# Kernel tuning notes

Measured on AMD Instinct MI355X. Metric: run time of the kernel, lower is better.

The kernel has to match this reference:

```python
import jax, jax.numpy as jnp
import numpy as np


def mish(x):
    return x * jnp.tanh(jax.nn.softplus(x))


def gcn(x, W, b, src, dst):
    # PyG GCNConv: h = D^-1/2 (A+I) D^-1/2 (x W) + b, aggregation at dst=edge_index[1]
    n = x.shape[0]
    h = x @ W
    deg = jax.ops.segment_sum(jnp.ones(src.shape[0], x.dtype), dst, num_segments=n) + 1.0
    dinv = jax.lax.rsqrt(deg)
    msg = h[src] * (dinv[src] * dinv[dst])[:, None]
    agg = jax.ops.segment_sum(msg, dst, num_segments=n)
    return agg + h * (dinv * dinv)[:, None] + b


def pool_mean(x, seg, num_segments):
    s = jax.ops.segment_sum(x, seg, num_segments=num_segments)
    c = jax.ops.segment_sum(jnp.ones(x.shape[0], x.dtype), seg, num_segments=num_segments)
    return s / jnp.maximum(c, 1.0)[:, None]


def attention(x, qW, qb, kW, kb, vW, vb, G):
    # x: [G*R, in_feats] -> per-graph self-attention over ROIs (dropout is identity in eval)
    R = x.shape[0] // G
    xc = x.reshape(G, R, x.shape[1])
    Q = xc @ qW + qb
    K = xc @ kW + kb
    Vv = xc @ vW + vb
    scores = jnp.einsum('gqd,gkd->gqk', Q, K) / (Q.shape[-1] ** 0.5)
    w = jax.nn.softmax(scores, axis=-1)
    out = jnp.einsum('gqk,gkd->gqd', w, Vv).reshape(G * R, Vv.shape[-1])
    return out, w.mean(axis=0)


def closs(a, b, temp=0.6):
    a = a / jnp.maximum(jnp.linalg.norm(a, axis=1, keepdims=True), 1e-12)
    b = b / jnp.maximum(jnp.linalg.norm(b, axis=1, keepdims=True), 1e-12)
    logits = (a @ b.T) / temp
    return -jnp.mean(jnp.diagonal(jax.nn.log_softmax(logits, axis=1)))


def setup_inputs() -> dict:
    key = jax.random.key(0)
    G, R1, R2, F_IN, H, OUT, DEG, V = 512, 200, 160, 128, 64, 64, 16, 64
    N1, N2 = G * R1, G * R2
    ks = iter(jax.random.split(key, 64))
    d = {}
    d['x1'] = jax.random.normal(next(ks), (N1, R1 + 3), jnp.float32)
    d['x2'] = jax.random.normal(next(ks), (N2, R2 + 3), jnp.float32)

    def lin(name, i, o):
        d[name + '_W'] = jax.random.normal(next(ks), (i, o), jnp.float32) * (i ** -0.5)
        d[name + '_b'] = jnp.zeros((o,), jnp.float32)

    lin('fcl', R1 + 3, F_IN); lin('fcr', R2 + 3, F_IN)
    lin('fcl1', R1, F_IN); lin('fcr1', R2, F_IN)
    lin('a1_q', F_IN, OUT); lin('a1_k', F_IN, OUT); lin('a1_v', F_IN, OUT)
    lin('a2_q', F_IN, OUT); lin('a2_k', F_IN, OUT); lin('a2_v', F_IN, OUT)
    lin('conv', F_IN, H); lin('conv1', H, H)
    lin('mlp', H, OUT)
    lin('fc1a', OUT * 4, F_IN); lin('fc1b', F_IN, 2)

    def edges(k, R):
        k1, k2 = jax.random.split(k)
        off = (jnp.arange(G, dtype=jnp.int32) * R)[:, None]
        src = jax.random.randint(k1, (G, R * DEG), 0, R, jnp.int32) + off
        dst = jax.random.randint(k2, (G, R * DEG), 0, R, jnp.int32) + off
        return jnp.stack([src.reshape(-1), dst.reshape(-1)])

    d['edge_index1'] = edges(next(ks), R1)
    d['edge_index2'] = edges(next(ks), R2)
    d['batch1'] = jnp.repeat(jnp.arange(G, dtype=jnp.int32), R1)
    d['batch2'] = jnp.repeat(jnp.arange(G, dtype=jnp.int32), R2)

    def sub(k, R):
        # one visited-node set (as in RW_subgraph) tiled per graph with offsets
        vis = jnp.sort(jax.random.permutation(k, R)[:V]).astype(jnp.int32)
        return (vis[None, :] + (jnp.arange(G, dtype=jnp.int32) * R)[:, None]).reshape(-1)

    d['sub_idx1'] = sub(next(ks), R1)
    d['sub_idx2'] = sub(next(ks), R2)
    d['num_graphs'] = G
    return d


def reference(x1, x2, fcl_W, fcl_b, fcr_W, fcr_b, fcl1_W, fcl1_b, fcr1_W, fcr1_b,
              a1_q_W, a1_q_b, a1_k_W, a1_k_b, a1_v_W, a1_v_b,
              a2_q_W, a2_q_b, a2_k_W, a2_k_b, a2_v_W, a2_v_b,
              conv_W, conv_b, conv1_W, conv1_b, mlp_W, mlp_b,
              fc1a_W, fc1a_b, fc1b_W, fc1b_b,
              edge_index1, edge_index2, batch1, batch2, sub_idx1, sub_idx2, num_graphs):
    G = int(num_graphs)
    src1, dst1 = edge_index1[0], edge_index1[1]
    src2, dst2 = edge_index2[0], edge_index2[1]

    z1 = x1[:, :-3] @ fcl1_W + fcl1_b
    z2 = x2[:, :-3] @ fcr1_W + fcr1_b
    z1, aw1 = attention(z1, a1_q_W, a1_q_b, a1_k_W, a1_k_b, a1_v_W, a1_v_b, G)
    z2, aw2 = attention(z2, a2_q_W, a2_q_b, a2_k_W, a2_k_b, a2_v_W, a2_v_b, G)
    z1 = pool_mean(z1, batch1, G)
    z2 = pool_mean(z2, batch2, G)

    h1 = x1 @ fcl_W + fcl_b
    h2 = x2 @ fcr_W + fcr_b
    o1 = mish(gcn(h1, conv_W, conv_b, src1, dst1))
    o2 = mish(gcn(h2, conv_W, conv_b, src2, dst2))
    o1 = gcn(o1, conv1_W, conv1_b, src1, dst1)
    o2 = gcn(o2, conv1_W, conv1_b, src2, dst2)

    s1 = o1[sub_idx1] @ mlp_W + mlp_b
    s2 = o2[sub_idx2] @ mlp_W + mlp_b
    s1 = pool_mean(s1, batch1[sub_idx1], G)
    s2 = pool_mean(s2, batch2[sub_idx2], G)

    c_loss = closs(s1, z2) + closs(z1, s2)
    feat = jnp.concatenate([s1, z1, s2, z2], axis=1)
    out = mish(feat @ fc1a_W + fc1a_b) @ fc1b_W + fc1b_b
    return c_loss, out, aw1, aw2
```

## Files before the change

kernel.cpp:

```cpp
#include <hip/hip_runtime.h>
#include <math.h>

#define TPB 256
#define MAXEP 4608

typedef float f32x4 __attribute__((ext_vector_type(4)));
typedef __bf16 bfv8 __attribute__((ext_vector_type(8)));

union U8 { uint4 q; unsigned short us[8]; __bf16 b[8]; bfv8 v; };

__device__ __forceinline__ unsigned short f2bfu(float f) {
  union { __bf16 h; unsigned short u; } x;
  x.h = (__bf16)f;
  return x.u;
}
__device__ __forceinline__ float bfu2f(unsigned short u) {
  return __uint_as_float((unsigned)u << 16);
}

__device__ __forceinline__ float mish_f(float x) {
  float sp = fmaxf(x, 0.f) + log1pf(expf(-fabsf(x)));
  return x * tanhf(sp);
}

__device__ __forceinline__ U8 loadA_f32(const float* Af, int kb, int K, bool rowok) {
  U8 u;
  if (rowok && kb + 8 <= K) {
    float4 f0 = *(const float4*)(Af + kb);
    float4 f1 = *(const float4*)(Af + kb + 4);
    u.b[0]=(__bf16)f0.x; u.b[1]=(__bf16)f0.y; u.b[2]=(__bf16)f0.z; u.b[3]=(__bf16)f0.w;
    u.b[4]=(__bf16)f1.x; u.b[5]=(__bf16)f1.y; u.b[6]=(__bf16)f1.z; u.b[7]=(__bf16)f1.w;
  } else {
#pragma unroll
    for (int j = 0; j < 8; ++j) {
      float f = (rowok && kb + j < K) ? Af[kb + j] : 0.f;
      u.b[j] = (__bf16)f;
    }
  }
  return u;
}

template<bool ABF16, bool CBF16, bool MISH, int NJ, int KPMAX, int RREP>
__global__ __launch_bounds__(256) void gemm2(
    const void* __restrict__ Av, const unsigned short* __restrict__ Bt,
    const float* __restrict__ bias, void* __restrict__ Cv,
    int N, int M, int K, int lda, int ldc,
    long sA, long sB, long sC, float alpha, int Kpad)
{
  constexpr int BM = NJ * 16;
  __shared__ unsigned short Bs[BM * KPMAX];

  const int tid = threadIdx.x;
  const int col0 = blockIdx.x * BM, row0 = blockIdx.y * 64 * RREP;

  {
    const unsigned short* Bp = Bt + (long)blockIdx.z * sB + (long)col0 * Kpad;
    int rows = M - col0; if (rows > BM) rows = BM;
    const int total = rows * Kpad;
    for (int i = tid * 8; i < total; i += TPB * 32) {
      uint4 a0, a1, a2, a3;
      bool b1 = i + TPB * 8  < total;
      bool b2 = i + TPB * 16 < total;
      bool b3 = i + TPB * 24 < total;
      a0 = *(const uint4*)&Bp[i];
      if (b1) a1 = *(const uint4*)&Bp[i + TPB * 8];
      if (b2) a2 = *(const uint4*)&Bp[i + TPB * 16];
      if (b3) a3 = *(const uint4*)&Bp[i + TPB * 24];
      *(uint4*)&Bs[i] = a0;
      if (b1) *(uint4*)&Bs[i + TPB * 8]  = a1;
      if (b2) *(uint4*)&Bs[i + TPB * 16] = a2;
      if (b3) *(uint4*)&Bs[i + TPB * 24] = a3;
    }
  }

  const int lane = tid & 63, w = tid >> 6;
  const int mrow = lane & 15, kg = lane >> 4;

  const unsigned short* Ah[RREP];
  const float* Af[RREP];
  bool rowok[RREP];
  U8 ua[RREP];
#pragma unroll
  for (int rr = 0; rr < RREP; ++rr) {
    int arow = row0 + rr * 64 + w * 16 + mrow;
    rowok[rr] = arow < N;
    if (ABF16) {
      Ah[rr] = (const unsigned short*)Av + (long)blockIdx.z * sA + (long)arow * lda;
      Af[rr] = nullptr;
      ua[rr].q = *(const uint4*)(Ah[rr] + kg * 8);
    } else {
      Af[rr] = (const float*)Av + (long)blockIdx.z * sA + (long)arow * lda;
      Ah[rr] = nullptr;
      ua[rr] = loadA_f32(Af[rr], kg * 8, K, rowok[rr]);
    }
  }

  __syncthreads();

  f32x4 acc[RREP][NJ];
#pragma unroll
  for (int rr = 0; rr < RREP; ++rr)
#pragma unroll
    for (int j = 0; j < NJ; ++j) acc[rr][j] = (f32x4)0.f;

  for (int k0 = 0; k0 < K; k0 += 32) {
    U8 un[RREP];
    bool more = (k0 + 32) < K;
    if (more) {
#pragma unroll
      for (int rr = 0; rr < RREP; ++rr) {
        if (ABF16) un[rr].q = *(const uint4*)(Ah[rr] + k0 + 32 + kg * 8);
        else       un[rr]   = loadA_f32(Af[rr], k0 + 32 + kg * 8, K, rowok[rr]);
      }
    }
    const int kb = k0 + kg * 8;
#pragma unroll
    for (int j = 0; j < NJ; ++j) {
      U8 ub;
      ub.q = *(const uint4*)&Bs[(j * 16 + mrow) * Kpad + kb];
#pragma unroll
      for (int rr = 0; rr < RREP; ++rr)
        acc[rr][j] = __builtin_amdgcn_mfma_f32_16x16x32_bf16(ua[rr].v, ub.v, acc[rr][j], 0, 0, 0);
    }
    if (more) {
#pragma unroll
      for (int rr = 0; rr < RREP; ++rr) ua[rr] = un[rr];
    }
  }

  long cbase = (long)blockIdx.z * sC;
#pragma unroll
  for (int rr = 0; rr < RREP; ++rr) {
#pragma unroll
    for (int j = 0; j < NJ; ++j) {
      int gc = col0 + j * 16 + mrow;
      if (gc >= M) continue;
      float bb = bias ? bias[gc] : 0.f;
#pragma unroll
      for (int r = 0; r < 4; ++r) {
        int gr = row0 + rr * 64 + w * 16 + kg * 4 + r;
        if (gr >= N) continue;
        float v = acc[rr][j][r] * alpha + bb;
        if (MISH) v = mish_f(v);
        if (CBF16) ((unsigned short*)Cv)[cbase + (long)gr * ldc + gc] = f2bfu(v);
        else       ((float*)Cv)[cbase + (long)gr * ldc + gc] = v;
      }
    }
  }
}

static inline int kpad_of(int K) { return ((K + 31) / 32) * 32 + 8; }

struct PrepSeg { const float* src; void* dst; int K, M, Kpad, kind; };
struct PrepArgs { PrepSeg s[19]; };

__global__ __launch_bounds__(256) void prep_weights(PrepArgs a) {
  PrepSeg sg = a.s[blockIdx.x];
  if (sg.kind == 0) {
    unsigned short* d = (unsigned short*)sg.dst;
    int tot = sg.M * sg.Kpad;
    for (int i = threadIdx.x; i < tot; i += TPB) {
      int m = i / sg.Kpad, k = i - m * sg.Kpad;
      float f = (k < sg.K) ? sg.src[(long)k * sg.M + m] : 0.f;
      d[i] = f2bfu(f);
    }
  } else if (sg.kind == 1) {
    float* d = (float*)sg.dst;
    for (int i = threadIdx.x; i < sg.K; i += TPB) d[i] = sg.src[i];
  } else {
    unsigned short* d = (unsigned short*)sg.dst;
    int tot = sg.M * sg.Kpad;
    for (int i = threadIdx.x; i < tot; i += TPB) {
      int m = i / sg.Kpad, k = i - m * sg.Kpad;
      float f = (k < sg.K) ? sg.src[(long)m * sg.K + k] : 0.f;
      d[i] = f2bfu(f);
    }
  }
}

__global__ __launch_bounds__(64) void bias_comb(const float* __restrict__ b_in,
                                                const unsigned short* __restrict__ Wt,
                                                int ldw, const float* __restrict__ bc,
                                                float* __restrict__ out, int M, int K)
{
  int m = blockIdx.x * 64 + threadIdx.x;
  if (m >= M) return;
  float s = bc ? bc[m] : 0.f;
  for (int k = 0; k < K; ++k) s += b_in[k] * bfu2f(Wt[(long)m * ldw + k]);
  out[m] = s;
}

__global__ __launch_bounds__(256) void ktvt2(
    const unsigned short* __restrict__ QKV, unsigned short* __restrict__ Kt,
    unsigned short* __restrict__ Vt, int R, int Rpad)
{
  __shared__ unsigned short tile[64][72];
  int g = blockIdx.x, tid = threadIdx.x;
  const unsigned short* q = QKV + (long)g * R * 192;
  unsigned short* kt = Kt + (long)g * R * 72;
  unsigned short* vt = Vt + (long)g * 64 * Rpad;

  {
    int c = tid & 63, w = tid >> 6;
    for (int r = w; r < R; r += 4)
      kt[r * 72 + c] = q[(long)r * 192 + 64 + c];
  }

  for (int r0 = 0; r0 < Rpad; r0 += 64) {
    __syncthreads();
    for (int i = tid; i < 64 * 64; i += TPB) {
      int rr = i >> 6, cc = i & 63;
      int r = r0 + rr;
      tile[cc][rr] = (r < R) ? q[(long)r * 192 + 128 + cc] : (unsigned short)0;
    }
    __syncthreads();
    int c = tid >> 2, j0 = (tid & 3) * 16;
    int lim = Rpad - r0; if (lim > 64) lim = 64;
    for (int jj = j0; jj < j0 + 16 && jj < lim; jj += 8) {
      uint4 qv = *(const uint4*)&tile[c][jj];
      *(uint4*)&vt[(long)c * Rpad + r0 + jj] = qv;
    }
  }
}

__global__ __launch_bounds__(256) void adj_build(
    const int* __restrict__ src, const int* __restrict__ dst,
    unsigned short* __restrict__ Adj, int R, int Rpad, int EPG)
{
  __shared__ float dinv_s[256];
  __shared__ unsigned short ssrc[MAXEP];
  __shared__ int cnt[256];
  __shared__ int scan[256];
  __shared__ int offx[257];
  __shared__ int cur[256];
  __shared__ float rowbuf[4][256];

  int g = blockIdx.x, tid = threadIdx.x;
  long ebase = (long)g * EPG;
  int gR = g * R;

  cnt[tid] = 0;
  __syncthreads();
  for (int e = tid; e < EPG; e += TPB)
    atomicAdd(&cnt[dst[ebase + e] - gR], 1);
  __syncthreads();

  int x = cnt[tid];
  int pc = (x + 7) & ~7;
  scan[tid] = pc;
  __syncthreads();
#pragma unroll
  for (int s = 1; s < 256; s <<= 1) {
    int t = (tid >= s) ? scan[tid - s] : 0;
    __syncthreads();
    scan[tid] += t;
    __syncthreads();
  }
  if (tid == 0) offx[0] = 0;
  offx[tid + 1] = scan[tid];
  cur[tid] = scan[tid] - pc;
  dinv_s[tid] = rsqrtf((float)x + 1.f);
  {
    unsigned dummy2 = 0xFFFFFFFFu;
    for (int i = tid; i < MAXEP / 2; i += TPB) ((unsigned*)ssrc)[i] = dummy2;
  }
  __syncthreads();

  for (int e = tid; e < EPG; e += TPB) {
    int d = dst[ebase + e] - gR;
    int s = src[ebase + e] - gR;
    int pos = atomicAdd(&cur[d], 1);
    ssrc[pos] = (unsigned short)s;
  }
  __syncthreads();

  int lane = tid & 63, w = tid >> 6;
  float* rb = rowbuf[w];
  for (int d = w; d < R; d += 4) {
#pragma unroll
    for (int i = 0; i < 4; ++i) rb[lane + i * 64] = 0.f;
    int i0 = offx[d], i1 = offx[d + 1];
    for (int i = i0 + lane; i < i1; i += 64) {
      int s = ssrc[i];
      if (s < R) atomicAdd(&rb[s], dinv_s[s]);
    }
    float dd = dinv_s[d];
    int c0 = lane * 4;
    if (c0 < Rpad) {
      ushort4 o;
      float v0 = rb[c0]     + (c0     == d ? dd : 0.f);
      float v1 = rb[c0 + 1] + (c0 + 1 == d ? dd : 0.f);
      float v2 = rb[c0 + 2] + (c0 + 2 == d ? dd : 0.f);
      float v3 = rb[c0 + 3] + (c0 + 3 == d ? dd : 0.f);
      o.x = f2bfu(v0 * dd); o.y = f2bfu(v1 * dd);
      o.z = f2bfu(v2 * dd); o.w = f2bfu(v3 * dd);
      *(ushort4*)&Adj[((long)gR + d) * Rpad + c0] = o;
    }
  }
}

__global__ __launch_bounds__(256) void transp64(
    const unsigned short* __restrict__ X, unsigned short* __restrict__ XT,
    int R, int Rpad)
{
  __shared__ unsigned short tile[64][72];
  int g = blockIdx.x, tid = threadIdx.x;
  const unsigned short* xg = X + (long)g * R * 64;
  unsigned short* xt = XT + (long)g * 64 * Rpad;
  for (int r0 = 0; r0 < Rpad; r0 += 64) {
    __syncthreads();
    for (int i = tid; i < 64 * 64; i += TPB) {
      int rr = i >> 6, cc = i & 63;
      int r = r0 + rr;
      tile[cc][rr] = (r < R) ? xg[(long)r * 64 + cc] : (unsigned short)0;
    }
    __syncthreads();
    int c = tid >> 2, j0 = (tid & 3) * 16;
    int lim = Rpad - r0; if (lim > 64) lim = 64;
    for (int jj = j0; jj < j0 + 16 && jj < lim; jj += 8) {
      uint4 q = *(const uint4*)&tile[c][jj];
      *(uint4*)&xt[(long)c * Rpad + r0 + jj] = q;
    }
  }
}

__global__ __launch_bounds__(256) void softmax_bf16(unsigned short* __restrict__ S,
                                                    int R, long rows)
{
  long wid = (long)blockIdx.x * 4 + (threadIdx.x >> 6);
  if (wid >= rows) return;
  int lane = threadIdx.x & 63;
  unsigned short* row = S + wid * R;
  float v[4];
  float mx = -1e30f;
#pragma unroll
  for (int t = 0; t < 4; ++t) {
    int j = lane + t * 64;
    v[t] = (j < R) ? bfu2f(row[j]) : -1e30f;
    mx = fmaxf(mx, v[t]);
  }
#pragma unroll
  for (int o = 32; o; o >>= 1) mx = fmaxf(mx, __shfl_xor(mx, o));
  float s = 0.f;
#pragma unroll
  for (int t = 0; t < 4; ++t) {
    int j = lane + t * 64;
    if (j < R) { v[t] = expf(v[t] - mx); s += v[t]; }
  }
#pragma unroll
  for (int o = 32; o; o >>= 1) s += __shfl_xor(s, o);
  float inv = 1.f / s;
#pragma unroll
  for (int t = 0; t < 4; ++t) {
    int j = lane + t * 64;
    if (j < R) row[j] = f2bfu(v[t] * inv);
  }
}

__global__ void meang_bf16(const unsigned short* __restrict__ S, float* __restrict__ out,
                           int RR, int G, float inv)
{
  int idx = blockIdx.x * TPB + threadIdx.x;
  if (idx >= RR) return;
  const unsigned short* p = S + idx;
  float s = 0.f;
  for (int g = 0; g + 8 <= G; g += 8) {
    s += bfu2f(p[(long)g * RR])       + bfu2f(p[(long)(g + 1) * RR]) +
         bfu2f(p[(long)(g + 2) * RR]) + bfu2f(p[(long)(g + 3) * RR]) +
         bfu2f(p[(long)(g + 4) * RR]) + bfu2f(p[(long)(g + 5) * RR]) +
         bfu2f(p[(long)(g + 6) * RR]) + bfu2f(p[(long)(g + 7) * RR]);
  }
  out[idx] = s * inv;
}

__global__ __launch_bounds__(256) void pool_mean_bf16(const unsigned short* __restrict__ X,
                                                      float* __restrict__ out, int R)
{
  __shared__ float part[4][64];
  int g = blockIdx.x, lane = threadIdx.x & 63, w = threadIdx.x >> 6;
  float s = 0.f;
  for (int r = w; r < R; r += 4)
    s += bfu2f(X[((long)g * R + r) * 64 + lane]);
  part[w][lane] = s;
  __syncthreads();
  if (w == 0)
    out[g * 64 + lane] = (part[0][lane] + part[1][lane] + part[2][lane] + part[3][lane]) * (1.f / R);
}

__global__ __launch_bounds__(64) void sub_mean_kernel(const unsigned short* __restrict__ X,
                                                      const int* __restrict__ sub,
                                                      float* __restrict__ out, int V)
{
  int g = blockIdx.x, lane = threadIdx.x;
  float s = 0.f;
  for (int v = 0; v + 4 <= V; v += 4) {
    int i0 = sub[g * V + v],     i1 = sub[g * V + v + 1];
    int i2 = sub[g * V + v + 2], i3 = sub[g * V + v + 3];
    s += bfu2f(X[(long)i0 * 64 + lane]) + bfu2f(X[(long)i1 * 64 + lane]) +
         bfu2f(X[(long)i2 * 64 + lane]) + bfu2f(X[(long)i3 * 64 + lane]);
  }
  out[g * 64 + lane] = s * (1.f / V);
}

__global__ __launch_bounds__(64) void norm_rows_kernel(const float* __restrict__ X,
                                                       float* __restrict__ Y)
{
  int g = blockIdx.x, lane = threadIdx.x;
  float x = X[g * 64 + lane];
  float ss = x * x;
#pragma unroll
  for (int o = 32; o; o >>= 1) ss += __shfl_xor(ss, o);
  float n = fmaxf(sqrtf(ss), 1e-12f);
  Y[g * 64 + lane] = x / n;
}

__global__ __launch_bounds__(256) void closs_kernel(const float* __restrict__ An,
                                                    const float* __restrict__ Bn,
                                                    float* __restrict__ loss, int G,
                                                    float invTemp, float coef)
{
  int i = blockIdx.x;
  __shared__ float arow[64];
  __shared__ float logits[512];
  __shared__ float red[256];
  int t = threadIdx.x;
  if (t < 64) arow[t] = An[i * 64 + t];
  __syncthreads();
  for (int j = t; j < G; j += 256) {
    const float* bp = Bn + (long)j * 64;
    float d = 0.f;
#pragma unroll
    for (int k = 0; k < 64; ++k) d = fmaf(arow[k], bp[k], d);
    logits[j] = d * invTemp;
  }
  __syncthreads();
  float mx = -1e30f;
  for (int j = t; j < G; j += 256) mx = fmaxf(mx, logits[j]);
  red[t] = mx; __syncthreads();
  for (int o = 128; o; o >>= 1) { if (t < o) red[t] = fmaxf(red[t], red[t + o]); __syncthreads(); }
  mx = red[0]; __syncthreads();
  float s = 0.f;
  for (int j = t; j < G; j += 256) s += expf(logits[j] - mx);
  red[t] = s; __syncthreads();
  for (int o = 128; o; o >>= 1) { if (t < o) red[t] += red[t + o]; __syncthreads(); }
  if (t == 0) {
    float lse = mx + logf(red[0]);
    atomicAdd(loss, coef * (lse - logits[i]));
  }
}

__global__ __launch_bounds__(128) void head_kernel(
    const float* __restrict__ s1, const float* __restrict__ z1,
    const float* __restrict__ s2, const float* __restrict__ z2,
    const float* __restrict__ W1, const float* __restrict__ b1,
    const float* __restrict__ W2, const float* __restrict__ b2,
    float* __restrict__ out)
{
  int g = blockIdx.x, t = threadIdx.x;
  __shared__ float feat[256];
  __shared__ float hid[128];
  if (t < 64) {
    feat[t]       = s1[g * 64 + t];
    feat[64 + t]  = z1[g * 64 + t];
    feat[128 + t] = s2[g * 64 + t];
    feat[192 + t] = z2[g * 64 + t];
  }
  __syncthreads();
  float acc = b1[t];
  for (int k = 0; k < 256; ++k) acc = fmaf(feat[k], W1[k * 128 + t], acc);
  hid[t] = mish_f(acc);
  __syncthreads();
  if (t < 2) {
    float a2 = b2[t];
#pragma unroll
    for (int k = 0; k < 128; ++k) a2 = fmaf(hid[k], W2[k * 2 + t], a2);
    out[g * 2 + t] = a2;
  }
}

#define LAUNCH_GEMM(ABF,CBF,MISH,NJ,KP,RREP, A,B,BI,C, N,M,K,LDA,LDC,SA,SB,SC,BAT,AL,KPAD) \
  { dim3 g_(((M)+(NJ)*16-1)/((NJ)*16), ((N)+(64*(RREP))-1)/(64*(RREP)), (BAT)); \
    gemm2<ABF,CBF,MISH,NJ,KP,RREP><<<g_,256,0,stream>>>((A),(B),(BI),(C),(N),(M),(K),(LDA),(LDC),(SA),(SB),(SC),(AL),(KPAD)); }

extern "C" void kernel_launch(void* const* d_in, const int* in_sizes, int n_in,
                              void* d_out, int out_size, void* d_ws, size_t ws_size,
                              hipStream_t stream)
{
  const float* x1     = (const float*)d_in[0];
  const float* x2     = (const float*)d_in[1];
  const float* fcl_W  = (const float*)d_in[2];  const float* fcl_b  = (const float*)d_in[3];
  const float* fcr_W  = (const float*)d_in[4];  const float* fcr_b  = (const float*)d_in[5];
  const float* fcl1_W = (const float*)d_in[6];  const float* fcl1_b = (const float*)d_in[7];
  const float* fcr1_W = (const float*)d_in[8];  const float* fcr1_b = (const float*)d_in[9];
  const float* a1qW = (const float*)d_in[10]; const float* a1qb = (const float*)d_in[11];
  const float* a1kW = (const float*)d_in[12]; const float* a1kb = (const float*)d_in[13];
  const float* a1vW = (const float*)d_in[14]; const float* a1vb = (const float*)d_in[15];
  const float* a2qW = (const float*)d_in[16]; const float* a2qb = (const float*)d_in[17];
  const float* a2kW = (const float*)d_in[18]; const float* a2kb = (const float*)d_in[19];
  const float* a2vW = (const float*)d_in[20]; const float* a2vb = (const float*)d_in[21];
  const float* convW  = (const float*)d_in[22]; const float* convb  = (const float*)d_in[23];
  const float* conv1W = (const float*)d_in[24]; const float* conv1b = (const float*)d_in[25];
  const float* mlpW   = (const float*)d_in[26]; const float* mlpb   = (const float*)d_in[27];
  const float* fc1aW  = (const float*)d_in[28]; const float* fc1ab  = (const float*)d_in[29];
  const float* fc1bW  = (const float*)d_in[30]; const float* fc1bb  = (const float*)d_in[31];
  const int* ei1  = (const int*)d_in[32];
  const int* ei2  = (const int*)d_in[33];
  const int* sub1 = (const int*)d_in[36];
  const int* sub2 = (const int*)d_in[37];

  const int R1 = in_sizes[6] / 128;
  const int R2 = in_sizes[8] / 128;
  const int N1 = in_sizes[34];
  const int N2 = in_sizes[35];
  const int G  = N1 / R1;
  const int E1 = in_sizes[32] / 2, E2 = in_sizes[33] / 2;
  const int EPG1 = E1 / G, EPG2 = E2 / G;
  const int V = in_sizes[36] / G;

  const int Kp1  = kpad_of(R1);
  const int Kp2  = kpad_of(R2);
  const int Kp1f = kpad_of(R1 + 3);
  const int Kp2f = kpad_of(R2 + 3);
  const int Rpad1 = Kp1, Rpad2 = Kp2;

  char* wp = (char*)d_ws;
  auto alloc = [&](size_t bytes) -> char* {
    char* p = wp; wp += (bytes + 255) & ~(size_t)255; return p;
  };
  size_t raSh = (size_t)G * R1 * R1;
  if ((size_t)N1 * 128 > raSh) raSh = (size_t)N1 * 128;
  unsigned short* RA = (unsigned short*)alloc(raSh * 2);
  unsigned short* RB = (unsigned short*)alloc((size_t)N1 * 192 * 2);
  unsigned short* Kt = (unsigned short*)alloc((size_t)G * R1 * 72 * 2);
  unsigned short* Vt = (unsigned short*)alloc((size_t)G * 64 * Rpad1 * 2);
  unsigned short* W5 = (unsigned short*)alloc((size_t)N1 * 64 * 2);
  unsigned short* Adj1 = (unsigned short*)alloc((size_t)G * R1 * Rpad1 * 2);
  unsigned short* Adj2 = (unsigned short*)alloc((size_t)G * R2 * Rpad2 * 2);
  unsigned short* fcl1n = (unsigned short*)alloc((size_t)R1 * 136 * 2);
  unsigned short* fcr1n = (unsigned short*)alloc((size_t)R2 * 136 * 2);
  unsigned short* fcln  = (unsigned short*)alloc((size_t)(R1 + 3) * 136 * 2);
  unsigned short* fcrn  = (unsigned short*)alloc((size_t)(R2 + 3) * 136 * 2);
  unsigned short* Wc1t   = (unsigned short*)alloc((size_t)192 * 136 * 2);
  unsigned short* Wc2t   = (unsigned short*)alloc((size_t)192 * 136 * 2);
  unsigned short* convt  = (unsigned short*)alloc((size_t)64 * 136 * 2);
  unsigned short* conv1t = (unsigned short*)alloc((size_t)64 * 72 * 2);
  unsigned short* mlpt   = (unsigned short*)alloc((size_t)64 * 72 * 2);
  size_t wzB1 = (size_t)192 * Kp1 * 2, wzB2 = (size_t)192 * Kp2 * 2;
  size_t wgB1 = (size_t)64 * Kp1f * 2, wgB2 = (size_t)64 * Kp2f * 2;
  char* comb = alloc(wzB1 + wzB2 + wgB1 + wgB2);
  unsigned short* Wz1t = (unsigned short*)comb;
  unsigned short* Wz2t = (unsigned short*)(comb + wzB1);
  unsigned short* Wg1t = (unsigned short*)(comb + wzB1 + wzB2);
  unsigned short* Wg2t = (unsigned short*)(comb + wzB1 + wzB2 + wgB1);
  float* bc1 = (float*)alloc(192 * 4);
  float* bc2 = (float*)alloc(192 * 4);
  float* bz1 = (float*)alloc(192 * 4);
  float* bz2 = (float*)alloc(192 * 4);
  float* bg1 = (float*)alloc(64 * 4);
  float* bg2 = (float*)alloc(64 * 4);
  float* Pz1 = (float*)alloc((size_t)G * 64 * 4);
  float* Pz2 = (float*)alloc((size_t)G * 64 * 4);
  float* Ps1 = (float*)alloc((size_t)G * 64 * 4);
  float* Ps2 = (float*)alloc((size_t)G * 64 * 4);
  float* Mt  = (float*)alloc((size_t)G * 64 * 4);
  float* n_s1 = (float*)alloc((size_t)G * 64 * 4);
  float* n_z2 = (float*)alloc((size_t)G * 64 * 4);
  float* n_z1 = (float*)alloc((size_t)G * 64 * 4);
  float* n_s2 = (float*)alloc((size_t)G * 64 * 4);
  (void)alloc(131072);

  float* loss = (float*)d_out;
  float* outp = loss + 1;
  float* aw1  = outp + (size_t)G * 2;
  float* aw2  = aw1 + (size_t)R1 * R1;

  hipMemsetAsync(d_out, 0, sizeof(float), stream);
  hipMemsetAsync(comb, 0, wzB1 + wzB2 + wgB1 + wgB2, stream);

  PrepArgs pa;
  int seg = 0;
  auto addp = [&](const float* s, unsigned short* d, int K, int M, int Kp, int kind) {
    pa.s[seg].src = s; pa.s[seg].dst = d; pa.s[seg].K = K; pa.s[seg].M = M;
    pa.s[seg].Kpad = Kp; pa.s[seg].kind = kind; seg++;
  };
  auto addb = [&](const float* s, float* d, int n) {
    pa.s[seg].src = s; pa.s[seg].dst = d; pa.s[seg].K = n; pa.s[seg].M = 0;
    pa.s[seg].Kpad = 0; pa.s[seg].kind = 1; seg++;
  };
  addp(fcl1_W, fcl1n, 128, R1, 136, 2);
  addp(fcr1_W, fcr1n, 128, R2, 136, 2);
  addp(fcl_W,  fcln,  128, R1 + 3, 136, 2);
  addp(fcr_W,  fcrn,  128, R2 + 3, 136, 2);
  addp(a1qW, Wc1t,             128, 64, 136, 0);
  addp(a1kW, Wc1t + 64 * 136,  128, 64, 136, 0);
  addp(a1vW, Wc1t + 128 * 136, 128, 64, 136, 0);
  addp(a2qW, Wc2t,             128, 64, 136, 0);
  addp(a2kW, Wc2t + 64 * 136,  128, 64, 136, 0);
  addp(a2vW, Wc2t + 128 * 136, 128, 64, 136, 0);
  addp(convW,  convt,  128, 64, 136, 0);
  addp(conv1W, conv1t, 64, 64, 72, 0);
  addp(mlpW,   mlpt,   64, 64, 72, 0);
  addb(a1qb, bc1, 64); addb(a1kb, bc1 + 64, 64); addb(a1vb, bc1 + 128, 64);
  addb(a2qb, bc2, 64); addb(a2kb, bc2 + 64, 64); addb(a2vb, bc2 + 128, 64);
  prep_weights<<<seg, 256, 0, stream>>>(pa);

  LAUNCH_GEMM(true, true, false, 8, 136, 1, Wc1t, fcl1n, nullptr, Wz1t,
              192, R1, 128, 136, Kp1, 0, 0, 0, 1, 1.f, 136);
  LAUNCH_GEMM(true, true, false, 8, 136, 1, Wc2t, fcr1n, nullptr, Wz2t,
              192, R2, 128, 136, Kp2, 0, 0, 0, 1, 1.f, 136);
  LAUNCH_GEMM(true, true, false, 8, 136, 1, convt, fcln, nullptr, Wg1t,
              64, R1 + 3, 128, 136, Kp1f, 0, 0, 0, 1, 1.f, 136);
  LAUNCH_GEMM(true, true, false, 8, 136, 1, convt, fcrn, nullptr, Wg2t,
              64, R2 + 3, 128, 136, Kp2f, 0, 0, 0, 1, 1.f, 136);
  bias_comb<<<3, 64, 0, stream>>>(fcl1_b, Wc1t, 136, bc1, bz1, 192, 128);
  bias_comb<<<3, 64, 0, stream>>>(fcr1_b, Wc2t, 136, bc2, bz2, 192, 128);
  bias_comb<<<1, 64, 0, stream>>>(fcl_b, convt, 136, nullptr, bg1, 64, 128);
  bias_comb<<<1, 64, 0, stream>>>(fcr_b, convt, 136, nullptr, bg2, 64, 128);

  LAUNCH_GEMM(false, true, false, 6, 232, 2, x1, Wz1t, bz1, RB,
              N1, 192, R1, R1 + 3, 192, 0, 0, 0, 1, 1.f, Kp1);
  ktvt2<<<G, 256, 0, stream>>>(RB, Kt, Vt, R1, Rpad1);
  LAUNCH_GEMM(true, true, false, 8, 72, 1, RB, Kt, nullptr, RA,
              R1, R1, 64, 192, R1, (long)R1 * 192, (long)R1 * 72, (long)R1 * R1,
              G, 0.125f, 72);
  {
    long rows = (long)G * R1;
    softmax_bf16<<<(int)((rows + 3) / 4), 256, 0, stream>>>(RA, R1, rows);
    meang_bf16<<<(R1 * R1 + TPB - 1) / TPB, TPB, 0, stream>>>(RA, aw1, R1 * R1, G, 1.f / G);
  }
  LAUNCH_GEMM(true, true, false, 4, 232, 1, RA, Vt, nullptr, W5,
              R1, 64, R1, R1, 64, (long)R1 * R1, (long)64 * Rpad1, (long)R1 * 64,
              G, 1.f, Rpad1);
  pool_mean_bf16<<<G, 256, 0, stream>>>(W5, Pz1, R1);

  LAUNCH_GEMM(false, true, false, 6, 232, 2, x2, Wz2t, bz2, RB,
              N2, 192, R2, R2 + 3, 192, 0, 0, 0, 1, 1.f, Kp2);
  ktvt2<<<G, 256, 0, stream>>>(RB, Kt, Vt, R2, Rpad2);
  LAUNCH_GEMM(true, true, false, 8, 72, 1, RB, Kt, nullptr, RA,
              R2, R2, 64, 192, R2, (long)R2 * 192, (long)R2 * 72, (long)R2 * R2,
              G, 0.125f, 72);
  {
    long rows = (long)G * R2;
    softmax_bf16<<<(int)((rows + 3) / 4), 256, 0, stream>>>(RA, R2, rows);
    meang_bf16<<<(R2 * R2 + TPB - 1) / TPB, TPB, 0, stream>>>(RA, aw2, R2 * R2, G, 1.f / G);
  }
  LAUNCH_GEMM(true, true, false, 4, 232, 1, RA, Vt, nullptr, W5,
              R2, 64, R2, R2, 64, (long)R2 * R2, (long)64 * Rpad2, (long)R2 * 64,
              G, 1.f, Rpad2);
  pool_mean_bf16<<<G, 256, 0, stream>>>(W5, Pz2, R2);

  unsigned short* hW0 = RB;
  unsigned short* hW1 = RB + (size_t)N1 * 64;
  unsigned short* hW2 = RB + (size_t)N1 * 128;
  LAUNCH_GEMM(false, true, false, 4, 232, 2, x1, Wg1t, bg1, hW0,
              N1, 64, R1 + 3, R1 + 3, 64, 0, 0, 0, 1, 1.f, Kp1f);
  adj_build<<<G, 256, 0, stream>>>(ei1, ei1 + E1, Adj1, R1, Rpad1, EPG1);
  transp64<<<G, 256, 0, stream>>>(hW0, Vt, R1, Rpad1);
  LAUNCH_GEMM(true, true, true, 4, 232, 1, Adj1, Vt, convb, hW1,
              R1, 64, R1, Rpad1, 64, (long)R1 * Rpad1, (long)64 * Rpad1, (long)R1 * 64,
              G, 1.f, Rpad1);
  LAUNCH_GEMM(true, true, false, 4, 136, 2, hW1, conv1t, nullptr, hW2,
              N1, 64, 64, 64, 64, 0, 0, 0, 1, 1.f, 72);
  transp64<<<G, 256, 0, stream>>>(hW2, Vt, R1, Rpad1);
  LAUNCH_GEMM(true, true, false, 4, 232, 1, Adj1, Vt, conv1b, hW0,
              R1, 64, R1, Rpad1, 64, (long)R1 * Rpad1, (long)64 * Rpad1, (long)R1 * 64,
              G, 1.f, Rpad1);
  sub_mean_kernel<<<G, 64, 0, stream>>>(hW0, sub1, Mt, V);
  LAUNCH_GEMM(false, false, false, 4, 136, 1, Mt, mlpt, mlpb, Ps1,
              G, 64, 64, 64, 64, 0, 0, 0, 1, 1.f, 72);

  LAUNCH_GEMM(false, true, false, 4, 232, 2, x2, Wg2t, bg2, hW0,
              N2, 64, R2 + 3, R2 + 3, 64, 0, 0, 0, 1, 1.f, Kp2f);
  adj_build<<<G, 256, 0, stream>>>(ei2, ei2 + E2, Adj2, R2, Rpad2, EPG2);
  transp64<<<G, 256, 0, stream>>>(hW0, Vt, R2, Rpad2);
  LAUNCH_GEMM(true, true, true, 4, 232, 1, Adj2, Vt, convb, hW1,
              R2, 64, R2, Rpad2, 64, (long)R2 * Rpad2, (long)64 * Rpad2, (long)R2 * 64,
              G, 1.f, Rpad2);
  LAUNCH_GEMM(true, true, false, 4, 136, 2, hW1, conv1t, nullptr, hW2,
              N2, 64, 64, 64, 64, 0, 0, 0, 1, 1.f, 72);
  transp64<<<G, 256, 0, stream>>>(hW2, Vt, R2, Rpad2);
  LAUNCH_GEMM(true, true, false, 4, 232, 1, Adj2, Vt, conv1b, hW0,
              R2, 64, R2, Rpad2, 64, (long)R2 * Rpad2, (long)64 * Rpad2, (long)R2 * 64,
              G, 1.f, Rpad2);
  sub_mean_kernel<<<G, 64, 0, stream>>>(hW0, sub2, Mt, V);
  LAUNCH_GEMM(false, false, false, 4, 136, 1, Mt, mlpt, mlpb, Ps2,
              G, 64, 64, 64, 64, 0, 0, 0, 1, 1.f, 72);

  norm_rows_kernel<<<G, 64, 0, stream>>>(Ps1, n_s1);
  norm_rows_kernel<<<G, 64, 0, stream>>>(Pz2, n_z2);
  norm_rows_kernel<<<G, 64, 0, stream>>>(Pz1, n_z1);
  norm_rows_kernel<<<G, 64, 0, stream>>>(Ps2, n_s2);
  const float invTemp = 1.f / 0.6f;
  closs_kernel<<<G, 256, 0, stream>>>(n_s1, n_z2, loss, G, invTemp, 1.f / G);
  closs_kernel<<<G, 256, 0, stream>>>(n_z1, n_s2, loss, G, invTemp, 1.f / G);

  head_kernel<<<G, 128, 0, stream>>>(Ps1, Pz1, Ps2, Pz2, fc1aW, fc1ab, fc1bW, fc1bb, outp);
}
```

Before: 965.7 us.

## Fuse attention QKV and GCN input projections into one 256-wide GEMM per branch

The two GEMMs that read x1 (and x2), one for the folded QKV projection and one for the GCN input projection, are merged into a single GEMM with a concatenated 256-column weight and bias. The output sits in a 256-wide buffer that ktvt2 and transp64 now read through a leading-dimension and column-offset argument. The aim is to read the large fp32 input matrices once per branch instead of twice and to launch fewer kernels. In exchange the kernel schedule is reordered, GCN branch 1 now runs before attention branch 2, the workspace needs an extra N1x256 buffer, and the first-layer GEMMs use a different per-block tiling parameter.

```diff
diff --git a/kernel.cpp b/kernel.cpp
--- a/kernel.cpp
+++ b/kernel.cpp
@@ -191,19 +191,19 @@
 }
 
 __global__ __launch_bounds__(256) void ktvt2(
-    const unsigned short* __restrict__ QKV, unsigned short* __restrict__ Kt,
-    unsigned short* __restrict__ Vt, int R, int Rpad)
+    const unsigned short* __restrict__ XO, unsigned short* __restrict__ Kt,
+    unsigned short* __restrict__ Vt, int R, int Rpad, int ld)
 {
   __shared__ unsigned short tile[64][72];
   int g = blockIdx.x, tid = threadIdx.x;
-  const unsigned short* q = QKV + (long)g * R * 192;
+  const unsigned short* q = XO + (long)g * R * ld;
   unsigned short* kt = Kt + (long)g * R * 72;
   unsigned short* vt = Vt + (long)g * 64 * Rpad;
 
   {
     int c = tid & 63, w = tid >> 6;
     for (int r = w; r < R; r += 4)
-      kt[r * 72 + c] = q[(long)r * 192 + 64 + c];
+      kt[r * 72 + c] = q[(long)r * ld + 64 + c];
   }
 
   for (int r0 = 0; r0 < Rpad; r0 += 64) {
@@ -211,7 +211,7 @@
     for (int i = tid; i < 64 * 64; i += TPB) {
       int rr = i >> 6, cc = i & 63;
       int r = r0 + rr;
-      tile[cc][rr] = (r < R) ? q[(long)r * 192 + 128 + cc] : (unsigned short)0;
+      tile[cc][rr] = (r < R) ? q[(long)r * ld + 128 + cc] : (unsigned short)0;
     }
     __syncthreads();
     int c = tid >> 2, j0 = (tid & 3) * 16;
@@ -301,18 +301,18 @@
 
 __global__ __launch_bounds__(256) void transp64(
     const unsigned short* __restrict__ X, unsigned short* __restrict__ XT,
-    int R, int Rpad)
+    int R, int Rpad, int ld, int coloff)
 {
   __shared__ unsigned short tile[64][72];
   int g = blockIdx.x, tid = threadIdx.x;
-  const unsigned short* xg = X + (long)g * R * 64;
+  const unsigned short* xg = X + (long)g * R * ld + coloff;
   unsigned short* xt = XT + (long)g * 64 * Rpad;
   for (int r0 = 0; r0 < Rpad; r0 += 64) {
     __syncthreads();
     for (int i = tid; i < 64 * 64; i += TPB) {
       int rr = i >> 6, cc = i & 63;
       int r = r0 + rr;
-      tile[cc][rr] = (r < R) ? xg[(long)r * 64 + cc] : (unsigned short)0;
+      tile[cc][rr] = (r < R) ? xg[(long)r * ld + cc] : (unsigned short)0;
     }
     __syncthreads();
     int c = tid >> 2, j0 = (tid & 3) * 16;
@@ -517,19 +517,18 @@
   const int EPG1 = E1 / G, EPG2 = E2 / G;
   const int V = in_sizes[36] / G;
 
-  const int Kp1  = kpad_of(R1);
-  const int Kp2  = kpad_of(R2);
   const int Kp1f = kpad_of(R1 + 3);
   const int Kp2f = kpad_of(R2 + 3);
-  const int Rpad1 = Kp1, Rpad2 = Kp2;
+  const int Rpad1 = kpad_of(R1);
+  const int Rpad2 = kpad_of(R2);
 
   char* wp = (char*)d_ws;
   auto alloc = [&](size_t bytes) -> char* {
     char* p = wp; wp += (bytes + 255) & ~(size_t)255; return p;
   };
   size_t raSh = (size_t)G * R1 * R1;
-  if ((size_t)N1 * 128 > raSh) raSh = (size_t)N1 * 128;
   unsigned short* RA = (unsigned short*)alloc(raSh * 2);
+  unsigned short* XO = (unsigned short*)alloc((size_t)N1 * 256 * 2);
   unsigned short* RB = (unsigned short*)alloc((size_t)N1 * 192 * 2);
   unsigned short* Kt = (unsigned short*)alloc((size_t)G * R1 * 72 * 2);
   unsigned short* Vt = (unsigned short*)alloc((size_t)G * 64 * Rpad1 * 2);
@@ -545,19 +544,14 @@
   unsigned short* convt  = (unsigned short*)alloc((size_t)64 * 136 * 2);
   unsigned short* conv1t = (unsigned short*)alloc((size_t)64 * 72 * 2);
   unsigned short* mlpt   = (unsigned short*)alloc((size_t)64 * 72 * 2);
-  size_t wzB1 = (size_t)192 * Kp1 * 2, wzB2 = (size_t)192 * Kp2 * 2;
-  size_t wgB1 = (size_t)64 * Kp1f * 2, wgB2 = (size_t)64 * Kp2f * 2;
-  char* comb = alloc(wzB1 + wzB2 + wgB1 + wgB2);
-  unsigned short* Wz1t = (unsigned short*)comb;
-  unsigned short* Wz2t = (unsigned short*)(comb + wzB1);
-  unsigned short* Wg1t = (unsigned short*)(comb + wzB1 + wzB2);
-  unsigned short* Wg2t = (unsigned short*)(comb + wzB1 + wzB2 + wgB1);
+  size_t wB1 = (size_t)256 * Kp1f * 2, wB2 = (size_t)256 * Kp2f * 2;
+  char* comb = alloc(wB1 + wB2);
+  unsigned short* Wzg1 = (unsigned short*)comb;
+  unsigned short* Wzg2 = (unsigned short*)(comb + wB1);
   float* bc1 = (float*)alloc(192 * 4);
   float* bc2 = (float*)alloc(192 * 4);
-  float* bz1 = (float*)alloc(192 * 4);
-  float* bz2 = (float*)alloc(192 * 4);
-  float* bg1 = (float*)alloc(64 * 4);
-  float* bg2 = (float*)alloc(64 * 4);
+  float* bzg1 = (float*)alloc(256 * 4);
+  float* bzg2 = (float*)alloc(256 * 4);
   float* Pz1 = (float*)alloc((size_t)G * 64 * 4);
   float* Pz2 = (float*)alloc((size_t)G * 64 * 4);
   float* Ps1 = (float*)alloc((size_t)G * 64 * 4);
@@ -575,7 +569,7 @@
   float* aw2  = aw1 + (size_t)R1 * R1;
 
   hipMemsetAsync(d_out, 0, sizeof(float), stream);
-  hipMemsetAsync(comb, 0, wzB1 + wzB2 + wgB1 + wgB2, stream);
+  hipMemsetAsync(comb, 0, wB1 + wB2, stream);
 
   PrepArgs pa;
   int seg = 0;
@@ -604,24 +598,28 @@
   addb(a2qb, bc2, 64); addb(a2kb, bc2 + 64, 64); addb(a2vb, bc2 + 128, 64);
   prep_weights<<<seg, 256, 0, stream>>>(pa);
 
-  LAUNCH_GEMM(true, true, false, 8, 136, 1, Wc1t, fcl1n, nullptr, Wz1t,
-              192, R1, 128, 136, Kp1, 0, 0, 0, 1, 1.f, 136);
-  LAUNCH_GEMM(true, true, false, 8, 136, 1, Wc2t, fcr1n, nullptr, Wz2t,
-              192, R2, 128, 136, Kp2, 0, 0, 0, 1, 1.f, 136);
-  LAUNCH_GEMM(true, true, false, 8, 136, 1, convt, fcln, nullptr, Wg1t,
+  LAUNCH_GEMM(true, true, false, 8, 136, 1, Wc1t, fcl1n, nullptr, Wzg1,
+              192, R1, 128, 136, Kp1f, 0, 0, 0, 1, 1.f, 136);
+  LAUNCH_GEMM(true, true, false, 8, 136, 1, convt, fcln, nullptr, Wzg1 + (size_t)192 * Kp1f,
               64, R1 + 3, 128, 136, Kp1f, 0, 0, 0, 1, 1.f, 136);
-  LAUNCH_GEMM(true, true, false, 8, 136, 1, convt, fcrn, nullptr, Wg2t,
+  LAUNCH_GEMM(true, true, false, 8, 136, 1, Wc2t, fcr1n, nullptr, Wzg2,
+              192, R2, 128, 136, Kp2f, 0, 0, 0, 1, 1.f, 136);
+  LAUNCH_GEMM(true, true, false, 8, 136, 1, convt, fcrn, nullptr, Wzg2 + (size_t)192 * Kp2f,
               64, R2 + 3, 128, 136, Kp2f, 0, 0, 0, 1, 1.f, 136);
-  bias_comb<<<3, 64, 0, stream>>>(fcl1_b, Wc1t, 136, bc1, bz1, 192, 128);
-  bias_comb<<<3, 64, 0, stream>>>(fcr1_b, Wc2t, 136, bc2, bz2, 192, 128);
-  bias_comb<<<1, 64, 0, stream>>>(fcl_b, convt, 136, nullptr, bg1, 64, 128);
-  bias_comb<<<1, 64, 0, stream>>>(fcr_b, convt, 136, nullptr, bg2, 64, 128);
-
-  LAUNCH_GEMM(false, true, false, 6, 232, 2, x1, Wz1t, bz1, RB,
-              N1, 192, R1, R1 + 3, 192, 0, 0, 0, 1, 1.f, Kp1);
-  ktvt2<<<G, 256, 0, stream>>>(RB, Kt, Vt, R1, Rpad1);
-  LAUNCH_GEMM(true, true, false, 8, 72, 1, RB, Kt, nullptr, RA,
-              R1, R1, 64, 192, R1, (long)R1 * 192, (long)R1 * 72, (long)R1 * R1,
+  bias_comb<<<3, 64, 0, stream>>>(fcl1_b, Wc1t, 136, bc1, bzg1, 192, 128);
+  bias_comb<<<1, 64, 0, stream>>>(fcl_b, convt, 136, nullptr, bzg1 + 192, 64, 128);
+  bias_comb<<<3, 64, 0, stream>>>(fcr1_b, Wc2t, 136, bc2, bzg2, 192, 128);
+  bias_comb<<<1, 64, 0, stream>>>(fcr_b, convt, 136, nullptr, bzg2 + 192, 64, 128);
+
+  unsigned short* hW1 = RB;
+  unsigned short* hW2 = RB + (size_t)N1 * 64;
+  unsigned short* hW3 = RB + (size_t)N1 * 128;
+
+  LAUNCH_GEMM(false, true, false, 4, 232, 2, x1, Wzg1, bzg1, XO,
+              N1, 256, R1 + 3, R1 + 3, 256, 0, 0, 0, 1, 1.f, Kp1f);
+  ktvt2<<<G, 256, 0, stream>>>(XO, Kt, Vt, R1, Rpad1, 256);
+  LAUNCH_GEMM(true, true, false, 8, 72, 1, XO, Kt, nullptr, RA,
+              R1, R1, 64, 256, R1, (long)R1 * 256, (long)R1 * 72, (long)R1 * R1,
               G, 0.125f, 72);
   {
     long rows = (long)G * R1;
@@ -632,12 +630,26 @@
               R1, 64, R1, R1, 64, (long)R1 * R1, (long)64 * Rpad1, (long)R1 * 64,
               G, 1.f, Rpad1);
   pool_mean_bf16<<<G, 256, 0, stream>>>(W5, Pz1, R1);
-
-  LAUNCH_GEMM(false, true, false, 6, 232, 2, x2, Wz2t, bz2, RB,
-              N2, 192, R2, R2 + 3, 192, 0, 0, 0, 1, 1.f, Kp2);
-  ktvt2<<<G, 256, 0, stream>>>(RB, Kt, Vt, R2, Rpad2);
-  LAUNCH_GEMM(true, true, false, 8, 72, 1, RB, Kt, nullptr, RA,
-              R2, R2, 64, 192, R2, (long)R2 * 192, (long)R2 * 72, (long)R2 * R2,
+  adj_build<<<G, 256, 0, stream>>>(ei1, ei1 + E1, Adj1, R1, Rpad1, EPG1);
+  transp64<<<G, 256, 0, stream>>>(XO, Vt, R1, Rpad1, 256, 192);
+  LAUNCH_GEMM(true, true, true, 4, 232, 1, Adj1, Vt, convb, hW1,
+              R1, 64, R1, Rpad1, 64, (long)R1 * Rpad1, (long)64 * Rpad1, (long)R1 * 64,
+              G, 1.f, Rpad1);
+  LAUNCH_GEMM(true, true, false, 4, 136, 2, hW1, conv1t, nullptr, hW2,
+              N1, 64, 64, 64, 64, 0, 0, 0, 1, 1.f, 72);
+  transp64<<<G, 256, 0, stream>>>(hW2, Vt, R1, Rpad1, 64, 0);
+  LAUNCH_GEMM(true, true, false, 4, 232, 1, Adj1, Vt, conv1b, hW3,
+              R1, 64, R1, Rpad1, 64, (long)R1 * Rpad1, (long)64 * Rpad1, (long)R1 * 64,
+              G, 1.f, Rpad1);
+  sub_mean_kernel<<<G, 64, 0, stream>>>(hW3, sub1, Mt, V);
+  LAUNCH_GEMM(false, false, false, 4, 136, 1, Mt, mlpt, mlpb, Ps1,
+              G, 64, 64, 64, 64, 0, 0, 0, 1, 1.f, 72);
+
+  LAUNCH_GEMM(false, true, false, 4, 232, 2, x2, Wzg2, bzg2, XO,
+              N2, 256, R2 + 3, R2 + 3, 256, 0, 0, 0, 1, 1.f, Kp2f);
+  ktvt2<<<G, 256, 0, stream>>>(XO, Kt, Vt, R2, Rpad2, 256);
+  LAUNCH_GEMM(true, true, false, 8, 72, 1, XO, Kt, nullptr, RA,
+              R2, R2, 64, 256, R2, (long)R2 * 256, (long)R2 * 72, (long)R2 * R2,
               G, 0.125f, 72);
   {
     long rows = (long)G * R2;
@@ -648,41 +660,18 @@
               R2, 64, R2, R2, 64, (long)R2 * R2, (long)64 * Rpad2, (long)R2 * 64,
               G, 1.f, Rpad2);
   pool_mean_bf16<<<G, 256, 0, stream>>>(W5, Pz2, R2);
-
-  unsigned short* hW0 = RB;
-  unsigned short* hW1 = RB + (size_t)N1 * 64;
-  unsigned short* hW2 = RB + (size_t)N1 * 128;
-  LAUNCH_GEMM(false, true, false, 4, 232, 2, x1, Wg1t, bg1, hW0,
-              N1, 64, R1 + 3, R1 + 3, 64, 0, 0, 0, 1, 1.f, Kp1f);
-  adj_build<<<G, 256, 0, stream>>>(ei1, ei1 + E1, Adj1, R1, Rpad1, EPG1);
-  transp64<<<G, 256, 0, stream>>>(hW0, Vt, R1, Rpad1);
-  LAUNCH_GEMM(true, true, true, 4, 232, 1, Adj1, Vt, convb, hW1,
-              R1, 64, R1, Rpad1, 64, (long)R1 * Rpad1, (long)64 * Rpad1, (long)R1 * 64,
-              G, 1.f, Rpad1);
-  LAUNCH_GEMM(true, true, false, 4, 136, 2, hW1, conv1t, nullptr, hW2,
-              N1, 64, 64, 64, 64, 0, 0, 0, 1, 1.f, 72);
-  transp64<<<G, 256, 0, stream>>>(hW2, Vt, R1, Rpad1);
-  LAUNCH_GEMM(true, true, false, 4, 232, 1, Adj1, Vt, conv1b, hW0,
-              R1, 64, R1, Rpad1, 64, (long)R1 * Rpad1, (long)64 * Rpad1, (long)R1 * 64,
-              G, 1.f, Rpad1);
-  sub_mean_kernel<<<G, 64, 0, stream>>>(hW0, sub1, Mt, V);
-  LAUNCH_GEMM(false, false, false, 4, 136, 1, Mt, mlpt, mlpb, Ps1,
-              G, 64, 64, 64, 64, 0, 0, 0, 1, 1.f, 72);
-
-  LAUNCH_GEMM(false, true, false, 4, 232, 2, x2, Wg2t, bg2, hW0,
-              N2, 64, R2 + 3, R2 + 3, 64, 0, 0, 0, 1, 1.f, Kp2f);
   adj_build<<<G, 256, 0, stream>>>(ei2, ei2 + E2, Adj2, R2, Rpad2, EPG2);
-  transp64<<<G, 256, 0, stream>>>(hW0, Vt, R2, Rpad2);
+  transp64<<<G, 256, 0, stream>>>(XO, Vt, R2, Rpad2, 256, 192);
   LAUNCH_GEMM(true, true, true, 4, 232, 1, Adj2, Vt, convb, hW1,
               R2, 64, R2, Rpad2, 64, (long)R2 * Rpad2, (long)64 * Rpad2, (long)R2 * 64,
               G, 1.f, Rpad2);
   LAUNCH_GEMM(true, true, false, 4, 136, 2, hW1, conv1t, nullptr, hW2,
               N2, 64, 64, 64, 64, 0, 0, 0, 1, 1.f, 72);
-  transp64<<<G, 256, 0, stream>>>(hW2, Vt, R2, Rpad2);
-  LAUNCH_GEMM(true, true, false, 4, 232, 1, Adj2, Vt, conv1b, hW0,
+  transp64<<<G, 256, 0, stream>>>(hW2, Vt, R2, Rpad2, 64, 0);
+  LAUNCH_GEMM(true, true, false, 4, 232, 1, Adj2, Vt, conv1b, hW3,
               R2, 64, R2, Rpad2, 64, (long)R2 * Rpad2, (long)64 * Rpad2, (long)R2 * 64,
               G, 1.f, Rpad2);
-  sub_mean_kernel<<<G, 64, 0, stream>>>(hW0, sub2, Mt, V);
+  sub_mean_kernel<<<G, 64, 0, stream>>>(hW3, sub2, Mt, V);
   LAUNCH_GEMM(false, false, false, 4, 136, 1, Mt, mlpt, mlpb, Ps2,
               G, 64, 64, 64, 64, 0, 0, 0, 1, 1.f, 72);
 
```

After: 1.004 ms. 3.9% more time.
